# Optimization experiments

Hardware: AMD Instinct MI355X
Metric: run time of the kernel (lower is better)

The kernel has to match this reference:

```python
import jax, jax.numpy as jnp
import numpy as np

B, N, CA, CS, CZ, H, NQ, NK = 2, 16384, 128, 128, 16, 4, 32, 128
DH = CA // H
NB = N // NQ


def _ln(x, gamma=None, eps=1e-5):
    m = jnp.mean(x, -1, keepdims=True)
    v = jnp.var(x, -1, keepdims=True)
    y = (x - m) * jax.lax.rsqrt(v + eps)
    return y if gamma is None else y * gamma


def _adaln(a, s, gamma_s, Wg, bg, Wskip):
    # AF3 Algorithm 26: LN(a) without affine; LN(s) with scale, no offset;
    # out = sigmoid(Linear(s)) * a + LinearNoBias(s)
    a_n = _ln(a)
    s_n = _ln(s, gamma_s)
    return jax.nn.sigmoid(s_n @ Wg + bg) * a_n + s_n @ Wskip


def setup_inputs():
    key = jax.random.key(0)
    ks = jax.random.split(key, 20)
    def nrm(i, shape, scale=0.02):
        return jax.random.normal(ks[i], shape, jnp.float32) * scale
    return {
        "a": jax.random.normal(ks[0], (B, N, CA), jnp.float32),
        "s": jax.random.normal(ks[1], (B, N, CS), jnp.float32),
        "z": jax.random.normal(ks[2], (B, NB, NQ, NK, CZ), jnp.float32),
        "apb_gamma_s": jnp.ones((CS,), jnp.float32),
        "apb_Wg": nrm(3, (CS, CA)),
        "apb_bg": jnp.zeros((CA,), jnp.float32),
        "apb_Wskip": nrm(4, (CS, CA)),
        "Wq": nrm(5, (CA, CA)), "bq": jnp.zeros((CA,), jnp.float32),
        "Wk": nrm(6, (CA, CA)), "Wv": nrm(7, (CA, CA)),
        "Wgate": nrm(8, (CA, CA)), "Wo": nrm(9, (CA, CA)),
        "gamma_z": jnp.ones((CZ,), jnp.float32),
        "Wz": nrm(10, (CZ, H)),
        "Ws_last": nrm(11, (CS, CA)),
        "bs_last": jnp.full((CA,), -2.0, jnp.float32),
        "ct_gamma_s": jnp.ones((CS,), jnp.float32),
        "ct_Wg": nrm(12, (CS, CA)), "ct_bg": jnp.zeros((CA,), jnp.float32),
        "ct_Wskip": nrm(13, (CS, CA)),
        "Wa1": nrm(14, (CA, 2 * CA)), "Wa2": nrm(15, (CA, 2 * CA)),
        "Wb": nrm(16, (2 * CA, CA)),
        "Ws": nrm(17, (CS, CA)), "bs": jnp.full((CA,), -2.0, jnp.float32),
        "n_queries": NQ, "n_keys": NK,
    }


def reference(a, s, z, apb_gamma_s, apb_Wg, apb_bg, apb_Wskip, Wq, bq, Wk, Wv,
              Wgate, Wo, gamma_z, Wz, Ws_last, bs_last, ct_gamma_s, ct_Wg,
              ct_bg, ct_Wskip, Wa1, Wa2, Wb, Ws, bs, n_queries, n_keys):
    nq, nk = int(n_queries), int(n_keys)
    nb = N // nq
    # ---- AttentionPairBias, local windowed attention ----
    a1 = _adaln(a, s, apb_gamma_s, apb_Wg, apb_bg, apb_Wskip)  # [B,N,CA]
    # trunked pair bias: [B,nb,nq,nk,H] -> [B,H,nb,nq,nk]
    bias = jnp.transpose(_ln(z, gamma_z) @ Wz, (0, 4, 1, 2, 3))
    q = (a1 @ Wq + bq).reshape(B, N, H, DH).transpose(0, 2, 1, 3)
    k = (a1 @ Wk).reshape(B, N, H, DH).transpose(0, 2, 1, 3)
    v = (a1 @ Wv).reshape(B, N, H, DH).transpose(0, 2, 1, 3)
    qb = q.reshape(B, H, nb, nq, DH)
    pad = (nk - nq) // 2
    # centered key window per query block
    idx = (jnp.arange(nb) * nq - pad)[:, None] + jnp.arange(nk)[None, :]  # [nb,nk]
    valid = (idx >= 0) & (idx < N)
    idxc = jnp.clip(idx, 0, N - 1)
    kb = k[:, :, idxc]  # [B,H,nb,nk,DH]
    vb = v[:, :, idxc]
    scores = jnp.einsum('bhnqd,bhnkd->bhnqk', qb, kb) / np.sqrt(DH).astype(np.float32) + bias
    scores = jnp.where(valid[None, None, :, None, :], scores, -1e9)
    attn = jax.nn.softmax(scores, axis=-1)
    o = jnp.einsum('bhnqk,bhnkd->bhnqd', attn, vb)  # [B,H,nb,nq,DH]
    o = o.reshape(B, H, N, DH).transpose(0, 2, 1, 3).reshape(B, N, CA)
    g = jax.nn.sigmoid(a1 @ Wgate)  # per-channel gating
    attn_out = (g * o) @ Wo
    b_out = jax.nn.sigmoid(s @ Ws_last + bs_last) * attn_out
    # ---- ConditionedTransitionBlock (Alg 25) ----
    a3 = _adaln(a, s, ct_gamma_s, ct_Wg, ct_bg, ct_Wskip)
    t = jax.nn.silu(a3 @ Wa1) * (a3 @ Wa2)
    ct_out = jax.nn.sigmoid(s @ Ws + bs) * (t @ Wb)
    # Alg 23: a = b + ConditionedTransitionBlock(a, s)
    return b_out + ct_out
```

## Files before the change

kernel.cpp:

```cpp
#include <hip/hip_runtime.h>

typedef _Float16 f16;
typedef f16 f16x8 __attribute__((ext_vector_type(8)));
typedef f16 f16x4 __attribute__((ext_vector_type(4)));
typedef float f32x4 __attribute__((ext_vector_type(4)));

#define MFMA16(a,b,c) __builtin_amdgcn_mfma_f32_16x16x32_f16((a),(b),(c),0,0,0)

static __device__ __forceinline__ f16x8 ld8(const f16* p){ return *(const f16x8*)p; }
static __device__ __forceinline__ float sigm(float x){ return 1.f/(1.f + __expf(-x)); }

__global__ __launch_bounds__(256) void k_prep(
    const float* __restrict__ apb_gamma, const float* __restrict__ apb_Wg, const float* __restrict__ apb_Wskip,
    const float* __restrict__ ct_gamma,  const float* __restrict__ ct_Wg,  const float* __restrict__ ct_Wskip,
    const float* __restrict__ Wq, const float* __restrict__ Wk, const float* __restrict__ Wv, const float* __restrict__ Wgate,
    const float* __restrict__ Wsl, const float* __restrict__ Wss,
    const float* __restrict__ Wa1, const float* __restrict__ Wa2,
    const float* __restrict__ Wo, const float* __restrict__ Wb,
    const float* __restrict__ gamma_z, const float* __restrict__ Wz,
    f16* __restrict__ wA, f16* __restrict__ wC, f16* __restrict__ wQK, f16* __restrict__ wVG,
    f16* __restrict__ wSG, f16* __restrict__ wAB, f16* __restrict__ wO, f16* __restrict__ wBt,
    float* __restrict__ wzg, float* __restrict__ Slv, float* __restrict__ Ssv)
{
  const int t0 = blockIdx.x*256 + threadIdx.x;
  const int stride = gridDim.x*256;
  for (int i = t0; i < 256*128; i += stride){
    const int n = i >> 7, k = i & 127;
    const int m = n & 127;
    wA[i]  = (f16)(((n<128) ? apb_Wg[k*128+m] : apb_Wskip[k*128+m]) * apb_gamma[k]);
    wC[i]  = (f16)(((n<128) ? ct_Wg[k*128+m]  : ct_Wskip[k*128+m])  * ct_gamma[k]);
    wQK[i] = (f16)((n<128) ? Wq[k*128+m] : Wk[k*128+m]);
    wVG[i] = (f16)((n<128) ? Wv[k*128+m] : Wgate[k*128+m]);
    wSG[i] = (f16)((n<128) ? Wsl[k*128+m] : Wss[k*128+m]);
  }
  for (int i = t0; i < 512*128; i += stride){
    const int n = i >> 7, k = i & 127;
    wAB[i] = (f16)((n < 256) ? Wa1[k*256 + n] : Wa2[k*256 + (n-256)]);
  }
  for (int i = t0; i < 128*128; i += stride){
    const int n = i >> 7, k = i & 127;
    wO[i] = (f16)Wo[k*128+n];
  }
  for (int i = t0; i < 128*256; i += stride){
    const int n = i >> 8, k = i & 255;
    wBt[i] = (f16)Wb[k*128+n];
  }
  if (t0 < 64) wzg[t0] = gamma_z[t0 & 15] * Wz[(t0 & 15)*4 + (t0 >> 4)];
  if (t0 < 1024){
    const int mat = t0 >> 9;
    const int j = t0 & 511;
    const int cc = j >> 2, part = j & 3;
    const float* Wp = mat ? Wss : Wsl;
    float acc = 0.f;
    #pragma unroll 4
    for (int k = part*32; k < part*32 + 32; k++) acc += Wp[k*128 + cc];
    acc += __shfl_xor(acc, 1);
    acc += __shfl_xor(acc, 2);
    if (part == 0){ if (mat) Ssv[cc] = acc; else Slv[cc] = acc; }
  }
}

__global__ __launch_bounds__(256, 4) void k_pre(
    const float* __restrict__ A, const float* __restrict__ S,
    const f16* __restrict__ wA, const f16* __restrict__ wC,
    const f16* __restrict__ wQK, const f16* __restrict__ wVG,
    const f16* __restrict__ wSG, const f16* __restrict__ wAB,
    const float* __restrict__ bgA, const float* __restrict__ bgC,
    const float* __restrict__ bq, const float* __restrict__ bsl, const float* __restrict__ bss,
    const float* __restrict__ Slv, const float* __restrict__ Ssv,
    f16* __restrict__ Qo, f16* __restrict__ Ko, f16* __restrict__ Vt, f16* __restrict__ Go,
    f16* __restrict__ T, f16* __restrict__ GL, f16* __restrict__ GS)
{
  __shared__ f16 lsn[32*136];
  __shared__ f16 lan[32*136];
  __shared__ f16 la1[32*136];
  __shared__ float lsm[32], lsd[32];
  const int tid = threadIdx.x;
  const size_t rbase = (size_t)blockIdx.x * 32;

  {
    const int half = tid >> 7;
    const int row = (tid & 127) >> 2, part = tid & 3;
    const size_t gr = rbase + row;
    const float* p = (half ? A : S) + gr*128 + part*32;
    float v[32];
    #pragma unroll
    for (int j = 0; j < 8; j++){
      const float4 t4 = ((const float4*)p)[j];
      v[j*4+0]=t4.x; v[j*4+1]=t4.y; v[j*4+2]=t4.z; v[j*4+3]=t4.w;
    }
    float sm = 0.f, sq = 0.f;
    #pragma unroll
    for (int j = 0; j < 32; j++){ sm += v[j]; sq += v[j]*v[j]; }
    sm += __shfl_xor(sm,1); sq += __shfl_xor(sq,1);
    sm += __shfl_xor(sm,2); sq += __shfl_xor(sq,2);
    const float mean = sm*(1.f/128.f);
    const float var  = sq*(1.f/128.f) - mean*mean;
    const float rstd = rsqrtf(var + 1e-5f);
    if (!half && part == 0){ lsm[row] = mean; lsd[row] = (var + 1e-5f)*rstd; }
    f16* dst = half ? lan : lsn;
    #pragma unroll
    for (int j = 0; j < 4; j++){
      f16x8 o;
      #pragma unroll
      for (int e = 0; e < 8; e++) o[e] = (f16)((v[j*8+e]-mean)*rstd);
      *(f16x8*)&dst[row*136 + part*32 + j*8] = o;
    }
  }
  __syncthreads();

  const int l = tid & 63, w = tid >> 6;
  const int c = l & 15, q4 = l >> 4;

  #pragma unroll
  for (int jj = 0; jj < 2; jj++){
    const int n0 = (jj*4 + w)*16;
    #pragma unroll
    for (int mat = 0; mat < 2; mat++){
      const f16* W = mat ? wC : wA;
      f16x8 b0[4], b1[4];
      #pragma unroll
      for (int kc = 0; kc < 4; kc++){
        b0[kc] = ld8(W + (size_t)(n0 + c)*128 + kc*32 + q4*8);
        b1[kc] = ld8(W + (size_t)(128 + n0 + c)*128 + kc*32 + q4*8);
      }
      const float4 bv = *(const float4*)((mat ? bgC : bgA) + n0 + q4*4);
      const float bvr[4] = {bv.x, bv.y, bv.z, bv.w};
      f16* dst = mat ? lan : la1;
      #pragma unroll
      for (int mi = 0; mi < 2; mi++){
        f32x4 d0 = {0,0,0,0}, d1 = {0,0,0,0};
        #pragma unroll
        for (int kc = 0; kc < 4; kc++){
          const f16x8 av = *(const f16x8*)&lsn[(mi*16 + c)*136 + kc*32 + q4*8];
          d0 = MFMA16(b0[kc], av, d0);
          d1 = MFMA16(b1[kc], av, d1);
        }
        const int row = mi*16 + c;
        const f16x4 anv = *(const f16x4*)&lan[row*136 + n0 + q4*4];
        f16x4 o;
        #pragma unroll
        for (int r = 0; r < 4; r++)
          o[r] = (f16)(sigm(d0[r] + bvr[r])*(float)anv[r] + d1[r]);
        *(f16x4*)&dst[row*136 + n0 + q4*4] = o;
      }
    }
  }
  __syncthreads();

  const int bidx = (int)(rbase >> 14);
  const int ntk0 = (int)(rbase & 16383);

  #pragma unroll
  for (int jj = 0; jj < 2; jj++){
    const int n0 = (jj*4 + w)*16;
    {
      f16x8 bQ[4], bK[4];
      #pragma unroll
      for (int kc = 0; kc < 4; kc++){
        bQ[kc] = ld8(wQK + (size_t)(n0 + c)*128 + kc*32 + q4*8);
        bK[kc] = ld8(wQK + (size_t)(128 + n0 + c)*128 + kc*32 + q4*8);
      }
      const float4 bv = *(const float4*)(bq + n0 + q4*4);
      const float bvr[4] = {bv.x, bv.y, bv.z, bv.w};
      #pragma unroll
      for (int mi = 0; mi < 2; mi++){
        f32x4 dQ = {0,0,0,0}, dK = {0,0,0,0};
        #pragma unroll
        for (int kc = 0; kc < 4; kc++){
          const f16x8 av = *(const f16x8*)&la1[(mi*16 + c)*136 + kc*32 + q4*8];
          dQ = MFMA16(bQ[kc], av, dQ);
          dK = MFMA16(bK[kc], av, dK);
        }
        const size_t grow = rbase + mi*16 + c;
        f16x4 qo, ko;
        #pragma unroll
        for (int r = 0; r < 4; r++){
          qo[r] = (f16)((dQ[r] + bvr[r])*0.17677669529663687f);
          ko[r] = (f16)dK[r];
        }
        *(f16x4*)&Qo[grow*128 + n0 + q4*4] = qo;
        *(f16x4*)&Ko[grow*128 + n0 + q4*4] = ko;
      }
    }
    {
      f16x8 bV[4], bG[4];
      #pragma unroll
      for (int kc = 0; kc < 4; kc++){
        bV[kc] = ld8(wVG + (size_t)(n0 + c)*128 + kc*32 + q4*8);
        bG[kc] = ld8(wVG + (size_t)(128 + n0 + c)*128 + kc*32 + q4*8);
      }
      #pragma unroll
      for (int mi = 0; mi < 2; mi++){
        f32x4 dV = {0,0,0,0}, dG = {0,0,0,0};
        #pragma unroll
        for (int kc = 0; kc < 4; kc++){
          const f16x8 av = *(const f16x8*)&la1[(mi*16 + c)*136 + kc*32 + q4*8];
          dV = MFMA16(av, bV[kc], dV);
          dG = MFMA16(bG[kc], av, dG);
        }
        const size_t grow = rbase + mi*16 + c;
        f16x4 go;
        #pragma unroll
        for (int r = 0; r < 4; r++) go[r] = (f16)sigm(dG[r]);
        *(f16x4*)&Go[grow*128 + n0 + q4*4] = go;
        f16x4 vv;
        #pragma unroll
        for (int r = 0; r < 4; r++) vv[r] = (f16)dV[r];
        *(f16x4*)(Vt + ((size_t)bidx*128 + n0 + c)*16384 + ntk0 + mi*16 + q4*4) = vv;
      }
    }
  }

  #pragma unroll
  for (int jj = 0; jj < 4; jj++){
    const int n0t = (jj*4 + w)*16;
    f16x8 b1v[4], b2v[4];
    #pragma unroll
    for (int kc = 0; kc < 4; kc++){
      b1v[kc] = ld8(wAB + (size_t)(n0t + c)*128 + kc*32 + q4*8);
      b2v[kc] = ld8(wAB + (size_t)(256 + n0t + c)*128 + kc*32 + q4*8);
    }
    #pragma unroll
    for (int mi = 0; mi < 2; mi++){
      f32x4 d0 = {0,0,0,0}, d1 = {0,0,0,0};
      #pragma unroll
      for (int kc = 0; kc < 4; kc++){
        const f16x8 av = *(const f16x8*)&lan[(mi*16 + c)*136 + kc*32 + q4*8];
        d0 = MFMA16(b1v[kc], av, d0);
        d1 = MFMA16(b2v[kc], av, d1);
      }
      const size_t grow = rbase + mi*16 + c;
      f16x4 t4;
      #pragma unroll
      for (int r = 0; r < 4; r++){
        const float u = d0[r];
        t4[r] = (f16)((u*sigm(u))*d1[r]);
      }
      *(f16x4*)&T[grow*256 + n0t + q4*4] = t4;
    }
  }

  #pragma unroll
  for (int jj = 0; jj < 2; jj++){
    const int n0 = (jj*4 + w)*16;
    f16x8 b0[4], b1[4];
    #pragma unroll
    for (int kc = 0; kc < 4; kc++){
      b0[kc] = ld8(wSG + (size_t)(n0 + c)*128 + kc*32 + q4*8);
      b1[kc] = ld8(wSG + (size_t)(128 + n0 + c)*128 + kc*32 + q4*8);
    }
    const float4 sl4 = *(const float4*)(Slv + n0 + q4*4);
    const float4 ss4 = *(const float4*)(Ssv + n0 + q4*4);
    const float4 bl4 = *(const float4*)(bsl + n0 + q4*4);
    const float4 bs4 = *(const float4*)(bss + n0 + q4*4);
    const float slr[4] = {sl4.x,sl4.y,sl4.z,sl4.w};
    const float ssr[4] = {ss4.x,ss4.y,ss4.z,ss4.w};
    const float blr[4] = {bl4.x,bl4.y,bl4.z,bl4.w};
    const float bsr[4] = {bs4.x,bs4.y,bs4.z,bs4.w};
    #pragma unroll
    for (int mi = 0; mi < 2; mi++){
      f32x4 d0 = {0,0,0,0}, d1 = {0,0,0,0};
      #pragma unroll
      for (int kc = 0; kc < 4; kc++){
        const f16x8 av = *(const f16x8*)&lsn[(mi*16 + c)*136 + kc*32 + q4*8];
        d0 = MFMA16(b0[kc], av, d0);
        d1 = MFMA16(b1[kc], av, d1);
      }
      const int row = mi*16 + c;
      const size_t grow = rbase + row;
      const float mn = lsm[row], sd = lsd[row];
      f16x4 gl4, gs4;
      #pragma unroll
      for (int r = 0; r < 4; r++){
        gl4[r] = (f16)sigm(d0[r]*sd + mn*slr[r] + blr[r]);
        gs4[r] = (f16)sigm(d1[r]*sd + mn*ssr[r] + bsr[r]);
      }
      *(f16x4*)&GL[grow*128 + n0 + q4*4] = gl4;
      *(f16x4*)&GS[grow*128 + n0 + q4*4] = gs4;
    }
  }
}

__global__ __launch_bounds__(512) void k_attn(const f16* __restrict__ Q, const f16* __restrict__ K,
    const f16* __restrict__ VT, const float* __restrict__ Z, const float* __restrict__ WZG,
    const f16* __restrict__ Go, const f16* __restrict__ T,
    const f16* __restrict__ Wot, const f16* __restrict__ Wbt,
    const f16* __restrict__ GL, const f16* __restrict__ GS, float* __restrict__ out)
{
  __shared__ f16 upb[17408];
  __shared__ float wzg_s[64];
  const int tid = threadIdx.x;
  const int b = blockIdx.x >> 9, nb = blockIdx.x & 511;
  if (tid < 64) wzg_s[tid] = WZG[tid];
  __syncthreads();
  #pragma unroll
  for (int i = 0; i < 8; i++){
    const int p  = tid + i*512;
    const int qq = p >> 7, kk = p & 127;
    const float* zp = Z + ((((size_t)b*512 + nb)*32 + qq)*128 + kk)*16;
    const float4 z0 = *(const float4*)(zp);
    const float4 z1 = *(const float4*)(zp + 4);
    const float4 z2 = *(const float4*)(zp + 8);
    const float4 z3 = *(const float4*)(zp + 12);
    const float xs[16] = {z0.x,z0.y,z0.z,z0.w, z1.x,z1.y,z1.z,z1.w,
                          z2.x,z2.y,z2.z,z2.w, z3.x,z3.y,z3.z,z3.w};
    float sm = 0.f, sq = 0.f;
    #pragma unroll
    for (int cc = 0; cc < 16; cc++){ sm += xs[cc]; sq += xs[cc]*xs[cc]; }
    const float mean = sm*(1.f/16.f);
    const float var  = sq*(1.f/16.f) - mean*mean;
    const float rs   = rsqrtf(var + 1e-5f);
    #pragma unroll
    for (int h = 0; h < 4; h++){
      float acc = 0.f;
      #pragma unroll
      for (int cc = 0; cc < 16; cc++) acc += (xs[cc]-mean)*wzg_s[h*16+cc];
      upb[(h*32 + qq)*132 + kk] = (f16)(acc*rs);
    }
  }
  __syncthreads();

  const int l = tid & 63, w = tid >> 6;
  const int c = l & 15, q4 = l >> 4;
  const int h = w >> 1, qh = w & 1, m0 = qh*16;
  const f16x8 qf = ld8(Q + ((size_t)b*16384 + (size_t)nb*32 + m0 + c)*128 + h*32 + q4*8);
  const long kbase = (long)b*16384 + (long)nb*32 - 48;
  f32x4 sc[8];
  #pragma unroll
  for (int nt = 0; nt < 8; nt++){
    const f16x8 kf = ld8(K + (kbase + nt*16 + c)*128 + h*32 + q4*8);
    f32x4 zz = {0.f,0.f,0.f,0.f};
    sc[nt] = MFMA16(kf, qf, zz);
  }
  #pragma unroll
  for (int nt = 0; nt < 8; nt++){
    const f16x4 bb = *(const f16x4*)&upb[(h*32 + m0 + c)*132 + nt*16 + q4*4];
    #pragma unroll
    for (int r = 0; r < 4; r++){
      const long kt = (long)nb*32 - 48 + nt*16 + q4*4 + r;
      const bool inv = (kt < 0) || (kt >= 16384);
      sc[nt][r] = inv ? -1e9f : (sc[nt][r] + (float)bb[r]);
    }
  }
  float mx = sc[0][0];
  #pragma unroll
  for (int nt = 0; nt < 8; nt++)
    #pragma unroll
    for (int r = 0; r < 4; r++) mx = fmaxf(mx, sc[nt][r]);
  mx = fmaxf(mx, __shfl_xor(mx, 16));
  mx = fmaxf(mx, __shfl_xor(mx, 32));
  float sum = 0.f;
  #pragma unroll
  for (int nt = 0; nt < 8; nt++)
    #pragma unroll
    for (int r = 0; r < 4; r++){ const float e = __expf(sc[nt][r]-mx); sc[nt][r] = e; sum += e; }
  sum += __shfl_xor(sum, 16);
  sum += __shfl_xor(sum, 32);
  const float inv = 1.f/sum;
  __syncthreads();
  #pragma unroll
  for (int nt = 0; nt < 8; nt++){
    f16x4 p4;
    #pragma unroll
    for (int r = 0; r < 4; r++) p4[r] = (f16)(sc[nt][r]*inv);
    *(f16x4*)&upb[(w*16 + c)*136 + nt*16 + q4*4] = p4;
  }
  const f16* vb = VT + ((long)b*128)*16384 + (long)nb*32 - 48;
  f32x4 o0 = {0.f,0.f,0.f,0.f}, o1 = {0.f,0.f,0.f,0.f};
  #pragma unroll
  for (int kc = 0; kc < 4; kc++){
    const f16x8 pa = *(const f16x8*)&upb[(w*16 + c)*136 + kc*32 + q4*8];
    const f16x8 v0 = ld8(vb + (long)(h*32 + c)*16384 + kc*32 + q4*8);
    const f16x8 v1 = ld8(vb + (long)(h*32 + 16 + c)*16384 + kc*32 + q4*8);
    o0 = MFMA16(pa, v0, o0);
    o1 = MFMA16(pa, v1, o1);
  }
  __syncthreads();
  #pragma unroll
  for (int r = 0; r < 4; r++){
    upb[(m0 + q4*4 + r)*140 + h*32 + c]      = (f16)o0[r];
    upb[(m0 + q4*4 + r)*140 + h*32 + 16 + c] = (f16)o1[r];
  }
  __syncthreads();

  const size_t tb = (size_t)b*16384 + (size_t)nb*32;
  #pragma unroll
  for (int mi = 0; mi < 2; mi++){
    const size_t tok = tb + mi*16 + c;
    f32x4 d1 = {0,0,0,0}, d2 = {0,0,0,0};
    #pragma unroll
    for (int kc = 0; kc < 4; kc++){
      const f16x8 gof = ld8(Go + tok*128 + kc*32 + q4*8) *
                        *(const f16x8*)&upb[(mi*16 + c)*140 + kc*32 + q4*8];
      d1 = MFMA16(ld8(Wot + (size_t)(w*16 + c)*128 + kc*32 + q4*8), gof, d1);
    }
    #pragma unroll
    for (int kc = 0; kc < 8; kc++)
      d2 = MFMA16(ld8(Wbt + (size_t)(w*16 + c)*256 + kc*32 + q4*8),
                  ld8(T + tok*256 + kc*32 + q4*8), d2);
    const f16x4 glv = *(const f16x4*)&GL[tok*128 + w*16 + q4*4];
    const f16x4 gsv = *(const f16x4*)&GS[tok*128 + w*16 + q4*4];
    float4 o;
    o.x = (float)glv[0]*d1[0] + (float)gsv[0]*d2[0];
    o.y = (float)glv[1]*d1[1] + (float)gsv[1]*d2[1];
    o.z = (float)glv[2]*d1[2] + (float)gsv[2]*d2[2];
    o.w = (float)glv[3]*d1[3] + (float)gsv[3]*d2[3];
    *(float4*)&out[tok*128 + w*16 + q4*4] = o;
  }
}

extern "C" void kernel_launch(void* const* d_in, const int* in_sizes, int n_in,
                              void* d_out, int out_size, void* d_ws, size_t ws_size,
                              hipStream_t stream)
{
  (void)in_sizes; (void)n_in; (void)out_size; (void)ws_size;
  const float* a        = (const float*)d_in[0];
  const float* s        = (const float*)d_in[1];
  const float* z        = (const float*)d_in[2];
  const float* apb_gamma= (const float*)d_in[3];
  const float* apb_Wg   = (const float*)d_in[4];
  const float* apb_bg   = (const float*)d_in[5];
  const float* apb_Wskip= (const float*)d_in[6];
  const float* Wq       = (const float*)d_in[7];
  const float* bq       = (const float*)d_in[8];
  const float* Wk       = (const float*)d_in[9];
  const float* Wv       = (const float*)d_in[10];
  const float* Wgate    = (const float*)d_in[11];
  const float* Wo       = (const float*)d_in[12];
  const float* gamma_z  = (const float*)d_in[13];
  const float* Wz       = (const float*)d_in[14];
  const float* Wsl      = (const float*)d_in[15];
  const float* bsl      = (const float*)d_in[16];
  const float* ct_gamma = (const float*)d_in[17];
  const float* ct_Wg    = (const float*)d_in[18];
  const float* ct_bg    = (const float*)d_in[19];
  const float* ct_Wskip = (const float*)d_in[20];
  const float* Wa1      = (const float*)d_in[21];
  const float* Wa2      = (const float*)d_in[22];
  const float* Wb       = (const float*)d_in[23];
  const float* Wss      = (const float*)d_in[24];
  const float* bss      = (const float*)d_in[25];

  f16* W0 = (f16*)d_ws;
  const size_t SL = (size_t)32768*128;
  f16* qv = W0 + 0*SL;
  f16* kv = W0 + 1*SL;
  f16* vt = W0 + 2*SL;
  f16* gv = W0 + 3*SL;
  f16* tv = W0 + 4*SL;
  f16* gl = W0 + 6*SL;
  f16* gs = W0 + 7*SL;
  f16* wA  = W0 + 8*SL;
  f16* wC  = wA  + 256*128;
  f16* wQK = wC  + 256*128;
  f16* wVG = wQK + 256*128;
  f16* wSG = wVG + 256*128;
  f16* wAB = wSG + 256*128;
  f16* wO  = wAB + 512*128;
  f16* wBt = wO  + 128*128;
  float* wzg = (float*)(wBt + 128*256);
  float* Slv = wzg + 64;
  float* Ssv = Slv + 128;

  k_prep<<<dim3(128),256,0,stream>>>(apb_gamma,apb_Wg,apb_Wskip, ct_gamma,ct_Wg,ct_Wskip,
      Wq,Wk,Wv,Wgate, Wsl,Wss, Wa1,Wa2, Wo,Wb, gamma_z,Wz,
      wA,wC,wQK,wVG,wSG,wAB,wO,wBt,wzg,Slv,Ssv);
  k_pre<<<dim3(1024),256,0,stream>>>(a,s, wA,wC,wQK,wVG,wSG,wAB,
      apb_bg,ct_bg,bq,bsl,bss,Slv,Ssv, qv,kv,vt,gv,tv,gl,gs);
  k_attn<<<dim3(1024),512,0,stream>>>(qv,kv,vt,z,wzg, gv,tv,wO,wBt,gl,gs,(float*)d_out);
}
```

Before: 558.1 us.

## Move pair-bias LayerNorm projection from attention kernel into interleaved pre-kernel blocks

The z-bias computation (LayerNorm over CZ plus projection to heads) moves out of k_attn into extra blocks of k_pre. Two of every three k_pre blocks now do bias work, interleaved with the projection blocks so the two streams of work can overlap. The bias is written to global memory as f16 and k_attn reads it directly, which removes the shared-memory staging and a barrier. In exchange there is an extra global write and read of the bias tensor, about 16 MB in f16, and k_pre's grid grows to 3072 blocks.

After: 629.3 us. +12.7%, slower.

```diff
diff --git a/kernel.cpp b/kernel.cpp
--- a/kernel.cpp
+++ b/kernel.cpp
@@ -62,6 +62,7 @@
 
 __global__ __launch_bounds__(256, 4) void k_pre(
     const float* __restrict__ A, const float* __restrict__ S,
+    const float* __restrict__ Z, const float* __restrict__ WZG,
     const f16* __restrict__ wA, const f16* __restrict__ wC,
     const f16* __restrict__ wQK, const f16* __restrict__ wVG,
     const f16* __restrict__ wSG, const f16* __restrict__ wAB,
@@ -69,14 +70,49 @@
     const float* __restrict__ bq, const float* __restrict__ bsl, const float* __restrict__ bss,
     const float* __restrict__ Slv, const float* __restrict__ Ssv,
     f16* __restrict__ Qo, f16* __restrict__ Ko, f16* __restrict__ Vt, f16* __restrict__ Go,
-    f16* __restrict__ T, f16* __restrict__ GL, f16* __restrict__ GS)
+    f16* __restrict__ T, f16* __restrict__ GL, f16* __restrict__ GS,
+    f16* __restrict__ BiasG)
 {
   __shared__ f16 lsn[32*136];
   __shared__ f16 lan[32*136];
   __shared__ f16 la1[32*136];
   __shared__ float lsm[32], lsd[32];
+  __shared__ float wzs[64];
   const int tid = threadIdx.x;
-  const size_t rbase = (size_t)blockIdx.x * 32;
+
+  if (blockIdx.x % 3 != 0){
+    const int bb = blockIdx.x - blockIdx.x/3 - 1;
+    if (tid < 64) wzs[tid] = WZG[tid];
+    __syncthreads();
+    #pragma unroll
+    for (int it = 0; it < 8; it++){
+      const int i = bb*2048 + it*256 + tid;
+      const float* zp = Z + (size_t)i*16;
+      const float4 z0 = *(const float4*)(zp);
+      const float4 z1 = *(const float4*)(zp + 4);
+      const float4 z2 = *(const float4*)(zp + 8);
+      const float4 z3 = *(const float4*)(zp + 12);
+      const float xs[16] = {z0.x,z0.y,z0.z,z0.w, z1.x,z1.y,z1.z,z1.w,
+                            z2.x,z2.y,z2.z,z2.w, z3.x,z3.y,z3.z,z3.w};
+      float sm = 0.f, sq = 0.f;
+      #pragma unroll
+      for (int cc = 0; cc < 16; cc++){ sm += xs[cc]; sq += xs[cc]*xs[cc]; }
+      const float mean = sm*(1.f/16.f);
+      const float var  = sq*(1.f/16.f) - mean*mean;
+      const float rs   = rsqrtf(var + 1e-5f);
+      const size_t tb4 = (size_t)(i >> 12) * 4;
+      const int qk = i & 4095;
+      #pragma unroll
+      for (int h = 0; h < 4; h++){
+        float acc = 0.f;
+        #pragma unroll
+        for (int cc = 0; cc < 16; cc++) acc += (xs[cc]-mean)*wzs[h*16+cc];
+        BiasG[(tb4 + h)*4096 + qk] = (f16)(acc*rs);
+      }
+    }
+    return;
+  }
+  const size_t rbase = (size_t)(blockIdx.x/3) * 32;
 
   {
     const int half = tid >> 7;
@@ -283,43 +319,14 @@
 }
 
 __global__ __launch_bounds__(512) void k_attn(const f16* __restrict__ Q, const f16* __restrict__ K,
-    const f16* __restrict__ VT, const float* __restrict__ Z, const float* __restrict__ WZG,
+    const f16* __restrict__ VT, const f16* __restrict__ BiasG,
     const f16* __restrict__ Go, const f16* __restrict__ T,
     const f16* __restrict__ Wot, const f16* __restrict__ Wbt,
     const f16* __restrict__ GL, const f16* __restrict__ GS, float* __restrict__ out)
 {
   __shared__ f16 upb[17408];
-  __shared__ float wzg_s[64];
   const int tid = threadIdx.x;
   const int b = blockIdx.x >> 9, nb = blockIdx.x & 511;
-  if (tid < 64) wzg_s[tid] = WZG[tid];
-  __syncthreads();
-  #pragma unroll
-  for (int i = 0; i < 8; i++){
-    const int p  = tid + i*512;
-    const int qq = p >> 7, kk = p & 127;
-    const float* zp = Z + ((((size_t)b*512 + nb)*32 + qq)*128 + kk)*16;
-    const float4 z0 = *(const float4*)(zp);
-    const float4 z1 = *(const float4*)(zp + 4);
-    const float4 z2 = *(const float4*)(zp + 8);
-    const float4 z3 = *(const float4*)(zp + 12);
-    const float xs[16] = {z0.x,z0.y,z0.z,z0.w, z1.x,z1.y,z1.z,z1.w,
-                          z2.x,z2.y,z2.z,z2.w, z3.x,z3.y,z3.z,z3.w};
-    float sm = 0.f, sq = 0.f;
-    #pragma unroll
-    for (int cc = 0; cc < 16; cc++){ sm += xs[cc]; sq += xs[cc]*xs[cc]; }
-    const float mean = sm*(1.f/16.f);
-    const float var  = sq*(1.f/16.f) - mean*mean;
-    const float rs   = rsqrtf(var + 1e-5f);
-    #pragma unroll
-    for (int h = 0; h < 4; h++){
-      float acc = 0.f;
-      #pragma unroll
-      for (int cc = 0; cc < 16; cc++) acc += (xs[cc]-mean)*wzg_s[h*16+cc];
-      upb[(h*32 + qq)*132 + kk] = (f16)(acc*rs);
-    }
-  }
-  __syncthreads();
 
   const int l = tid & 63, w = tid >> 6;
   const int c = l & 15, q4 = l >> 4;
@@ -333,9 +340,10 @@
     f32x4 zz = {0.f,0.f,0.f,0.f};
     sc[nt] = MFMA16(kf, qf, zz);
   }
+  const f16* bt = BiasG + (((size_t)(b*512 + nb)*4 + h)*32 + m0 + c)*128;
   #pragma unroll
   for (int nt = 0; nt < 8; nt++){
-    const f16x4 bb = *(const f16x4*)&upb[(h*32 + m0 + c)*132 + nt*16 + q4*4];
+    const f16x4 bb = *(const f16x4*)&bt[nt*16 + q4*4];
     #pragma unroll
     for (int r = 0; r < 4; r++){
       const long kt = (long)nb*32 - 48 + nt*16 + q4*4 + r;
@@ -358,7 +366,6 @@
   sum += __shfl_xor(sum, 16);
   sum += __shfl_xor(sum, 32);
   const float inv = 1.f/sum;
-  __syncthreads();
   #pragma unroll
   for (int nt = 0; nt < 8; nt++){
     f16x4 p4;
@@ -451,7 +458,8 @@
   f16* tv = W0 + 4*SL;
   f16* gl = W0 + 6*SL;
   f16* gs = W0 + 7*SL;
-  f16* wA  = W0 + 8*SL;
+  f16* biasG = W0 + 8*SL;
+  f16* wA  = W0 + 12*SL;
   f16* wC  = wA  + 256*128;
   f16* wQK = wC  + 256*128;
   f16* wVG = wQK + 256*128;
@@ -466,7 +474,7 @@
   k_prep<<<dim3(128),256,0,stream>>>(apb_gamma,apb_Wg,apb_Wskip, ct_gamma,ct_Wg,ct_Wskip,
       Wq,Wk,Wv,Wgate, Wsl,Wss, Wa1,Wa2, Wo,Wb, gamma_z,Wz,
       wA,wC,wQK,wVG,wSG,wAB,wO,wBt,wzg,Slv,Ssv);
-  k_pre<<<dim3(1024),256,0,stream>>>(a,s, wA,wC,wQK,wVG,wSG,wAB,
-      apb_bg,ct_bg,bq,bsl,bss,Slv,Ssv, qv,kv,vt,gv,tv,gl,gs);
-  k_attn<<<dim3(1024),512,0,stream>>>(qv,kv,vt,z,wzg, gv,tv,wO,wBt,gl,gs,(float*)d_out);
+  k_pre<<<dim3(3072),256,0,stream>>>(a,s, z,wzg, wA,wC,wQK,wVG,wSG,wAB,
+      apb_bg,ct_bg,bq,bsl,bss,Slv,Ssv, qv,kv,vt,gv,tv,gl,gs, biasG);
+  k_attn<<<dim3(1024),512,0,stream>>>(qv,kv,vt,biasG, gv,tv,wO,wBt,gl,gs,(float*)d_out);
 }
```
